# Kernel optimization log

Hardware: AMD Instinct MI355X
Metric: run time of the kernel (lower is better)

The kernel has to match this reference:

```python
import jax, jax.numpy as jnp
import numpy as np

B, S, E, H = 4, 2048, 768, 12
D = E // H  # head_dim = 64


def setup_inputs() -> dict:
    key = jax.random.key(0)
    k1, k2, k3 = jax.random.split(key, 3)
    x = jax.random.normal(k1, (B, S, E), dtype=jnp.float32)
    # torch Linear(E, 3E): weight [3E, E]; we store transposed [E, 3E] for x @ W
    W_qkv = jax.random.normal(k2, (E, 3 * E), dtype=jnp.float32) * (E ** -0.5)
    b_qkv = jax.random.normal(k3, (3 * E,), dtype=jnp.float32) * 0.02
    return {"x": x, "W_qkv": W_qkv, "b_qkv": b_qkv}


def reference(x, W_qkv, b_qkv):
    n, length, embed_dim = x.shape
    qkv = x @ W_qkv + b_qkv                                   # [B, S, 3E]
    qkv = qkv.reshape(n, length, 3, H, D).transpose(2, 0, 3, 1, 4)  # [3, B, H, S, D]
    q, k, v = qkv[0], qkv[1], qkv[2]
    scores = jnp.einsum('bhsd,bhtd->bhst', q, k) * (D ** -0.5)  # [B, H, S, S]
    attn = jax.nn.softmax(scores, axis=-1)
    out = jnp.einsum('bhst,bhtd->bhsd', attn, v)               # [B, H, S, D]
    return out.transpose(0, 2, 1, 3).reshape(n, length, embed_dim)
```

## Files before the change

### kernel.cpp

```cpp
#include <hip/hip_runtime.h>
#include <cmath>

#define B_ 4
#define S_ 2048
#define E_ 768
#define H_ 12
#define D_ 64
#define NE3 (3*E_)
#define QKV_ELEMS ((size_t)B_*H_*S_*D_)

typedef __attribute__((ext_vector_type(8)))  short bf16x8;
typedef __attribute__((ext_vector_type(4)))  float f32x4;
typedef __attribute__((ext_vector_type(16))) float f32x16;

__device__ __forceinline__ unsigned short f2bf(float f) {
    union { float f; unsigned u; } v; v.f = f;
    return (unsigned short)((v.u + 0x7FFFu + ((v.u >> 16) & 1u)) >> 16);
}
__device__ __forceinline__ float exp2_fast(float x) {
    float r; asm("v_exp_f32 %0, %1" : "=v"(r) : "v"(x)); return r;
}
__device__ __forceinline__ float max3f(float a, float b, float c) {
    float r; asm("v_max3_f32 %0, %1, %2, %3" : "=v"(r) : "v"(a), "v"(b), "v"(c));
    return r;
}
#define LOG2E 1.44269504088896340736f

__global__ __launch_bounds__(256)
void cvt_x(const float* __restrict__ x, unsigned short* __restrict__ xb)
{
    const size_t i = ((size_t)blockIdx.x * 256 + threadIdx.x) * 8;
    float4 a = *(const float4*)(x + i);
    float4 b = *(const float4*)(x + i + 4);
    ushort4 o0, o1;
    o0.x = f2bf(a.x); o0.y = f2bf(a.y); o0.z = f2bf(a.z); o0.w = f2bf(a.w);
    o1.x = f2bf(b.x); o1.y = f2bf(b.y); o1.z = f2bf(b.z); o1.w = f2bf(b.w);
    *(ushort4*)(xb + i)     = o0;
    *(ushort4*)(xb + i + 4) = o1;
}

__global__ __launch_bounds__(256)
void transpose_w(const float* __restrict__ W, unsigned short* __restrict__ Wt)
{
    __shared__ float t[32][33];
    const int tx = threadIdx.x & 31;
    const int ty = threadIdx.x >> 5;
    const int n0 = blockIdx.x * 32;
    const int k0 = blockIdx.y * 32;
    #pragma unroll
    for (int r = 0; r < 4; ++r)
        t[ty + 8*r][tx] = W[(size_t)(k0 + ty + 8*r) * NE3 + n0 + tx];
    __syncthreads();
    #pragma unroll
    for (int r = 0; r < 4; ++r)
        Wt[(size_t)(n0 + ty + 8*r) * E_ + k0 + tx] = f2bf(t[tx][ty + 8*r]);
}

__global__ __launch_bounds__(256, 2)
void qkv_gemm_mfma(const unsigned short* __restrict__ xb,
                   const unsigned short* __restrict__ Wt,
                   const float* __restrict__ bias,
                   unsigned short* __restrict__ qkv)
{
    __shared__ __align__(16) unsigned short As[128*64];
    __shared__ __align__(16) unsigned short Bs[128*64];

    const int tid  = threadIdx.x;
    const int lane = tid & 63;
    const int wave = tid >> 6;
    const int lo   = lane & 15;
    const int hi   = lane >> 4;
    const int wr   = wave >> 1;
    const int wc   = wave & 1;
    const int nstart = blockIdx.x * 128;
    const int mstart = blockIdx.y * 128;

    f32x4 acc[4][4];
    #pragma unroll
    for (int i = 0; i < 4; ++i)
        #pragma unroll
        for (int j = 0; j < 4; ++j) acc[i][j] = (f32x4){0.f,0.f,0.f,0.f};

    for (int k0 = 0; k0 < E_; k0 += 64) {
        __syncthreads();
        #pragma unroll
        for (int it = 0; it < 4; ++it) {
            const int cid = tid + it*256;
            const int row = cid >> 3, c = cid & 7;
            bf16x8 av = *(const bf16x8*)(xb + (size_t)(mstart + row)*E_ + k0 + c*8);
            *(bf16x8*)&As[row*64 + ((c ^ (row & 7)) * 8)] = av;
            bf16x8 bv = *(const bf16x8*)(Wt + (size_t)(nstart + row)*E_ + k0 + c*8);
            *(bf16x8*)&Bs[row*64 + ((c ^ (row & 7)) * 8)] = bv;
        }
        __syncthreads();

        #pragma unroll
        for (int ks = 0; ks < 2; ++ks) {
            const int c = ks*4 + hi;
            bf16x8 af[4], bfr[4];
            #pragma unroll
            for (int i = 0; i < 4; ++i) {
                const int ar = wr*64 + i*16 + lo;
                af[i] = *(const bf16x8*)&As[ar*64 + ((c ^ (ar & 7)) * 8)];
            }
            #pragma unroll
            for (int j = 0; j < 4; ++j) {
                const int br = wc*64 + j*16 + lo;
                bfr[j] = *(const bf16x8*)&Bs[br*64 + ((c ^ (br & 7)) * 8)];
            }
            #pragma unroll
            for (int i = 0; i < 4; ++i)
                #pragma unroll
                for (int j = 0; j < 4; ++j)
                    acc[i][j] = __builtin_amdgcn_mfma_f32_16x16x32_bf16(
                        af[i], bfr[j], acc[i][j], 0, 0, 0);
        }
    }

    #pragma unroll
    for (int j = 0; j < 4; ++j) {
        const int ncol = nstart + wc*64 + j*16 + lo;
        const int g  = ncol >> 6;
        const int cq = g / H_;
        const int h  = g % H_;
        const int d  = ncol & 63;
        const float bv = bias[ncol];
        const float qscale = (cq == 0) ? 0.125f : 1.0f;
        unsigned short* dst = qkv + (size_t)cq * QKV_ELEMS;
        #pragma unroll
        for (int i = 0; i < 4; ++i) {
            const int mbase = mstart + wr*64 + i*16 + hi*4;
            #pragma unroll
            for (int r = 0; r < 4; ++r) {
                const int m = mbase + r;
                const int b = m >> 11;
                const int s = m & 2047;
                dst[(((size_t)(b*H_ + h))*S_ + s)*D_ + d] =
                    f2bf((acc[i][j][r] + bv) * qscale);
            }
        }
    }
}

__global__ __launch_bounds__(256, 2)
void attn_mfma32(const unsigned short* __restrict__ qkv, float* __restrict__ out)
{
    __shared__ __align__(16) unsigned short Ks[2*64*64];
    __shared__ __align__(16) unsigned short Vt[2*64*64];

    const int tid  = threadIdx.x;
    const int lane = tid & 63;
    const int wave = tid >> 6;
    const int q32  = lane & 31;
    const int hi   = lane >> 5;
    const int qtile = blockIdx.x * 128;
    const int bh = blockIdx.y;
    const size_t base = (size_t)bh * S_ * D_;

    const unsigned short* Q = qkv;
    const unsigned short* K = qkv + QKV_ELEMS;
    const unsigned short* V = qkv + 2*QKV_ELEMS;

    bf16x8 qf[4];
    {
        const size_t qrow = base + (size_t)(qtile + wave*32 + q32) * D_;
        #pragma unroll
        for (int m = 0; m < 4; ++m)
            qf[m] = *(const bf16x8*)(Q + qrow + m*16 + hi*8);
    }

    const int kkey0 = tid >> 3,          kch0 = tid & 7;
    const int kkey1 = (tid + 256) >> 3,  kch1 = (tid + 256) & 7;

    bf16x8 kreg0, kreg1, vreg0, vreg1;
    #define LOADKV(kc_) do {                                                         \
        kreg0 = *(const bf16x8*)(K + base + (size_t)((kc_) + kkey0)*D_ + kch0*8);    \
        kreg1 = *(const bf16x8*)(K + base + (size_t)((kc_) + kkey1)*D_ + kch1*8);    \
        vreg0 = *(const bf16x8*)(V + base + (size_t)((kc_) + lane)*D_ + wave*16);    \
        vreg1 = *(const bf16x8*)(V + base + (size_t)((kc_) + lane)*D_ + wave*16 + 8);\
    } while (0)
    #define STOREKV(buf_) do {                                                       \
        const int o_ = (buf_) * 4096;                                                \
        *(bf16x8*)&Ks[o_ + kkey0*64 + ((kch0 ^ (kkey0 & 7)) * 8)] = kreg0;           \
        *(bf16x8*)&Ks[o_ + kkey1*64 + ((kch1 ^ (kkey1 & 7)) * 8)] = kreg1;           \
        _Pragma("unroll")                                                            \
        for (int j = 0; j < 8; ++j) {                                                \
            const int d = wave*16 + j;                                               \
            Vt[o_ + d*64 + (((lane >> 3) ^ (d & 7)) * 8) + (lane & 7)] =             \
                (unsigned short)vreg0[j];                                            \
        }                                                                            \
        _Pragma("unroll")                                                            \
        for (int j = 0; j < 8; ++j) {                                                \
            const int d = wave*16 + 8 + j;                                           \
            Vt[o_ + d*64 + (((lane >> 3) ^ (d & 7)) * 8) + (lane & 7)] =             \
                (unsigned short)vreg1[j];                                            \
        }                                                                            \
    } while (0)

    f32x16 o0, o1;
    #pragma unroll
    for (int r = 0; r < 16; ++r) { o0[r] = 0.f; o1[r] = 0.f; }
    float m_run = -INFINITY, l_run = 0.f;

    LOADKV(0);
    STOREKV(0);
    __syncthreads();
    int cur = 0;

    for (int kc = 0; kc < S_; kc += 64) {
        const int nkc = (kc + 64 < S_) ? (kc + 64) : 0;
        LOADKV(nkc);

        const int o = cur * 4096;

        f32x16 sg[2];
        __builtin_amdgcn_s_setprio(1);
        #pragma unroll
        for (int g = 0; g < 2; ++g) {
            f32x16 acc;
            #pragma unroll
            for (int r = 0; r < 16; ++r) acc[r] = 0.f;
            const int key = g*32 + q32;
            #pragma unroll
            for (int m = 0; m < 4; ++m) {
                const int c = m*2 + hi;
                bf16x8 kf = *(const bf16x8*)&Ks[o + key*64 + ((c ^ (key & 7)) * 8)];
                acc = __builtin_amdgcn_mfma_f32_32x32x16_bf16(kf, qf[m], acc, 0, 0, 0);
            }
            sg[g] = acc;
        }
        __builtin_amdgcn_s_setprio(0);

        float m0 = fmaxf(sg[0][0], sg[0][1]);
        float m1 = fmaxf(sg[0][8], sg[0][9]);
        float m2 = fmaxf(sg[1][0], sg[1][1]);
        float m3 = fmaxf(sg[1][8], sg[1][9]);
        #pragma unroll
        for (int r = 2; r < 8; r += 2) {
            m0 = max3f(m0, sg[0][r],   sg[0][r+1]);
            m1 = max3f(m1, sg[0][r+8], sg[0][r+9]);
            m2 = max3f(m2, sg[1][r],   sg[1][r+1]);
            m3 = max3f(m3, sg[1][r+8], sg[1][r+9]);
        }
        float mx = fmaxf(fmaxf(m0, m1), fmaxf(m2, m3));
        mx = fmaxf(mx, __shfl_xor(mx, 32));
        const float mn    = fmaxf(m_run, mx);
        const float alpha = exp2_fast((m_run - mn) * LOG2E);
        m_run = mn;
        const float nmnL = -mn * LOG2E;

        #pragma unroll
        for (int r = 0; r < 16; ++r) sg[0][r] = exp2_fast(fmaf(sg[0][r], LOG2E, nmnL));
        #pragma unroll
        for (int r = 0; r < 16; ++r) sg[1][r] = exp2_fast(fmaf(sg[1][r], LOG2E, nmnL));

        float a8[8];
        #pragma unroll
        for (int r = 0; r < 8; ++r) a8[r] = (sg[0][r] + sg[0][r+8]) + (sg[1][r] + sg[1][r+8]);
        float a4_0 = a8[0] + a8[4], a4_1 = a8[1] + a8[5];
        float a4_2 = a8[2] + a8[6], a4_3 = a8[3] + a8[7];
        float psum = (a4_0 + a4_1) + (a4_2 + a4_3);
        psum += __shfl_xor(psum, 32);
        l_run = l_run * alpha + psum;

        #pragma unroll
        for (int r = 0; r < 16; ++r) { o0[r] *= alpha; o1[r] *= alpha; }

        unsigned U0[8], U1[8];
        #pragma unroll
        for (int c2 = 0; c2 < 8; ++c2) {
            asm("v_cvt_pk_bf16_f32 %0, %1, %2"
                : "=v"(U0[c2]) : "v"(sg[0][2*c2]), "v"(sg[0][2*c2+1]));
            asm("v_cvt_pk_bf16_f32 %0, %1, %2"
                : "=v"(U1[c2]) : "v"(sg[1][2*c2]), "v"(sg[1][2*c2+1]));
        }

        unsigned R0[2][2], R1[2][2];
        #pragma unroll
        for (int tb = 0; tb < 2; ++tb)
            #pragma unroll
            for (int w2 = 0; w2 < 2; ++w2) {
                unsigned s0 = hi ? U0[4*tb + w2] : U0[4*tb + 2 + w2];
                unsigned s1 = hi ? U1[4*tb + w2] : U1[4*tb + 2 + w2];
                R0[tb][w2] = (unsigned)__shfl_xor((int)s0, 32);
                R1[tb][w2] = (unsigned)__shfl_xor((int)s1, 32);
            }

        __builtin_amdgcn_s_setprio(1);
        #pragma unroll
        for (int t = 0; t < 4; ++t) {
            const int tb = t & 1;
            union { unsigned w[4]; bf16x8 v; } pw;
            if (t < 2) {
                pw.w[0] = hi ? R0[tb][0] : U0[4*tb + 0];
                pw.w[1] = hi ? R0[tb][1] : U0[4*tb + 1];
                pw.w[2] = hi ? U0[4*tb + 2] : R0[tb][0];
                pw.w[3] = hi ? U0[4*tb + 3] : R0[tb][1];
            } else {
                pw.w[0] = hi ? R1[tb][0] : U1[4*tb + 0];
                pw.w[1] = hi ? R1[tb][1] : U1[4*tb + 1];
                pw.w[2] = hi ? U1[4*tb + 2] : R1[tb][0];
                pw.w[3] = hi ? U1[4*tb + 3] : R1[tb][1];
            }
            const int c = t*2 + hi;
            {
                const int d = q32;
                bf16x8 vf = *(const bf16x8*)&Vt[o + d*64 + ((c ^ (d & 7)) * 8)];
                o0 = __builtin_amdgcn_mfma_f32_32x32x16_bf16(vf, pw.v, o0, 0, 0, 0);
            }
            {
                const int d = 32 + q32;
                bf16x8 vf = *(const bf16x8*)&Vt[o + d*64 + ((c ^ (d & 7)) * 8)];
                o1 = __builtin_amdgcn_mfma_f32_32x32x16_bf16(vf, pw.v, o1, 0, 0, 0);
            }
        }
        __builtin_amdgcn_s_setprio(0);

        STOREKV(cur ^ 1);
        __syncthreads();
        cur ^= 1;
    }

    const int b = bh / H_;
    const int h = bh % H_;
    const float inv = 1.f / l_run;
    const int qglob = qtile + wave*32 + q32;
    float* obase = out + ((size_t)b*S_ + qglob)*E_ + h*64;
    #pragma unroll
    for (int rg = 0; rg < 4; ++rg) {
        float4 w0 = { o0[4*rg+0]*inv, o0[4*rg+1]*inv, o0[4*rg+2]*inv, o0[4*rg+3]*inv };
        *(float4*)(obase + rg*8 + hi*4) = w0;
        float4 w1 = { o1[4*rg+0]*inv, o1[4*rg+1]*inv, o1[4*rg+2]*inv, o1[4*rg+3]*inv };
        *(float4*)(obase + 32 + rg*8 + hi*4) = w1;
    }
    #undef LOADKV
    #undef STOREKV
}

extern "C" void kernel_launch(void* const* d_in, const int* in_sizes, int n_in,
                              void* d_out, int out_size, void* d_ws, size_t ws_size,
                              hipStream_t stream)
{
    (void)in_sizes; (void)n_in; (void)out_size; (void)ws_size;
    const float* x    = (const float*)d_in[0];
    const float* W    = (const float*)d_in[1];
    const float* bias = (const float*)d_in[2];
    float* out = (float*)d_out;

    unsigned short* qkv = (unsigned short*)d_ws;
    unsigned short* xb  = qkv + 3*QKV_ELEMS;
    unsigned short* Wtb = xb + (size_t)B_*S_*E_;

    cvt_x<<<(B_*S_*E_)/(256*8), 256, 0, stream>>>(x, xb);
    transpose_w<<<dim3(NE3/32, E_/32), 256, 0, stream>>>(W, Wtb);

    dim3 g1(NE3/128, (B_*S_)/128);
    qkv_gemm_mfma<<<g1, 256, 0, stream>>>(xb, Wtb, bias, qkv);

    dim3 g2(S_/128, B_*H_);
    attn_mfma32<<<g2, 256, 0, stream>>>(qkv, out);
}
```

Before: 138.3 us.

## Load K tiles directly to LDS and skip softmax rescale unless max grows

K tiles now go straight from global memory into LDS with global_load_lds, with the swizzle moved to the source address, so the register staging and ds_write step for K is gone. The online-softmax rescale of the output accumulators and running sum is skipped unless the row maximum grows by more than a threshold (FA4-style lazy rescaling). This removes per-iteration multiplies, but exponentials can now run on a stale maximum (bounded by 2^(8*log2e)). The direct-to-LDS load may also need a different wait/sync pattern to be ordered correctly against the barrier.

```diff
diff --git a/kernel.cpp b/kernel.cpp
--- a/kernel.cpp
+++ b/kernel.cpp
@@ -172,17 +172,25 @@
     const int kkey0 = tid >> 3,          kch0 = tid & 7;
     const int kkey1 = (tid + 256) >> 3,  kch1 = (tid + 256) & 7;
 
-    bf16x8 kreg0, kreg1, vreg0, vreg1;
-    #define LOADKV(kc_) do {                                                         \
-        kreg0 = *(const bf16x8*)(K + base + (size_t)((kc_) + kkey0)*D_ + kch0*8);    \
-        kreg1 = *(const bf16x8*)(K + base + (size_t)((kc_) + kkey1)*D_ + kch1*8);    \
+    bf16x8 vreg0, vreg1;
+    #define GLOADK(kc_, buf_) do {                                                   \
+        __builtin_amdgcn_global_load_lds(                                            \
+            (const __attribute__((address_space(1))) unsigned*)                      \
+                (K + base + (size_t)((kc_) + kkey0)*D_ + ((kch0 ^ (kkey0 & 7))*8)),  \
+            (__attribute__((address_space(3))) unsigned*)&Ks[(buf_)*4096 + tid*8],   \
+            16, 0, 0);                                                               \
+        __builtin_amdgcn_global_load_lds(                                            \
+            (const __attribute__((address_space(1))) unsigned*)                      \
+                (K + base + (size_t)((kc_) + kkey1)*D_ + ((kch1 ^ (kkey1 & 7))*8)),  \
+            (__attribute__((address_space(3))) unsigned*)&Ks[(buf_)*4096 + (tid+256)*8], \
+            16, 0, 0);                                                               \
+    } while (0)
+    #define LOADV(kc_) do {                                                          \
         vreg0 = *(const bf16x8*)(V + base + (size_t)((kc_) + lane)*D_ + wave*16);    \
         vreg1 = *(const bf16x8*)(V + base + (size_t)((kc_) + lane)*D_ + wave*16 + 8);\
     } while (0)
-    #define STOREKV(buf_) do {                                                       \
+    #define STOREV(buf_) do {                                                        \
         const int o_ = (buf_) * 4096;                                                \
-        *(bf16x8*)&Ks[o_ + kkey0*64 + ((kch0 ^ (kkey0 & 7)) * 8)] = kreg0;           \
-        *(bf16x8*)&Ks[o_ + kkey1*64 + ((kch1 ^ (kkey1 & 7)) * 8)] = kreg1;           \
         _Pragma("unroll")                                                            \
         for (int j = 0; j < 8; ++j) {                                                \
             const int d = wave*16 + j;                                               \
@@ -202,14 +210,16 @@
     for (int r = 0; r < 16; ++r) { o0[r] = 0.f; o1[r] = 0.f; }
     float m_run = -INFINITY, l_run = 0.f;
 
-    LOADKV(0);
-    STOREKV(0);
+    GLOADK(0, 0);
+    LOADV(0);
+    STOREV(0);
     __syncthreads();
     int cur = 0;
 
     for (int kc = 0; kc < S_; kc += 64) {
         const int nkc = (kc + 64 < S_) ? (kc + 64) : 0;
-        LOADKV(nkc);
+        GLOADK(nkc, cur ^ 1);
+        LOADV(nkc);
 
         const int o = cur * 4096;
 
@@ -244,10 +254,16 @@
         }
         float mx = fmaxf(fmaxf(m0, m1), fmaxf(m2, m3));
         mx = fmaxf(mx, __shfl_xor(mx, 32));
-        const float mn    = fmaxf(m_run, mx);
-        const float alpha = exp2_fast((m_run - mn) * LOG2E);
-        m_run = mn;
-        const float nmnL = -mn * LOG2E;
+
+        if (__any(mx > m_run + 8.0f)) {
+            const float mn    = fmaxf(m_run, mx);
+            const float alpha = exp2_fast((m_run - mn) * LOG2E);
+            m_run = mn;
+            l_run *= alpha;
+            #pragma unroll
+            for (int r = 0; r < 16; ++r) { o0[r] *= alpha; o1[r] *= alpha; }
+        }
+        const float nmnL = -m_run * LOG2E;
 
         #pragma unroll
         for (int r = 0; r < 16; ++r) sg[0][r] = exp2_fast(fmaf(sg[0][r], LOG2E, nmnL));
@@ -261,10 +277,7 @@
         float a4_2 = a8[2] + a8[6], a4_3 = a8[3] + a8[7];
         float psum = (a4_0 + a4_1) + (a4_2 + a4_3);
         psum += __shfl_xor(psum, 32);
-        l_run = l_run * alpha + psum;
-
-        #pragma unroll
-        for (int r = 0; r < 16; ++r) { o0[r] *= alpha; o1[r] *= alpha; }
+        l_run += psum;
 
         unsigned U0[8], U1[8];
         #pragma unroll
@@ -316,7 +329,7 @@
         }
         __builtin_amdgcn_s_setprio(0);
 
-        STOREKV(cur ^ 1);
+        STOREV(cur ^ 1);
         __syncthreads();
         cur ^= 1;
     }
@@ -333,8 +346,9 @@
         float4 w1 = { o1[4*rg+0]*inv, o1[4*rg+1]*inv, o1[4*rg+2]*inv, o1[4*rg+3]*inv };
         *(float4*)(obase + 32 + rg*8 + hi*4) = w1;
     }
-    #undef LOADKV
-    #undef STOREKV
+    #undef GLOADK
+    #undef LOADV
+    #undef STOREV
 }
 
 extern "C" void kernel_launch(void* const* d_in, const int* in_sizes, int n_in,
```

After: 138.4 us. About the same (+0.1%).
